# Performance work log

Measured on AMD Instinct MI355X. Metric: run time of the kernel, lower is better.

Reference implementation:

```python
import jax, jax.numpy as jnp
import numpy as np

B, S, D, H, MLP, RH, RANK, BS, E, RES = 64, 197, 768, 12, 3072, 512, 256, 2, 3, 1
EPS = 1e-5


def _ln(x, g, b):
    m = jnp.mean(x, -1, keepdims=True)
    v = jnp.mean((x - m) ** 2, -1, keepdims=True)
    return (x - m) / jnp.sqrt(v + EPS) * g + b


def setup_inputs() -> dict:
    key = jax.random.key(0)
    ks = jax.random.split(key, 16)
    n = lambda k, shp, s: (jax.random.normal(k, shp) * s).astype(jnp.float32)
    inp = {
        'x': n(ks[0], (B, S, D), 1.0),
        'LRA_mask': jnp.arange(2 ** BS, dtype=jnp.int32),
        'wq_w': n(ks[1], (D, D), 0.02), 'wq_b': jnp.zeros((D,), jnp.float32),
        'wk_w': n(ks[2], (D, D), 0.02), 'wk_b': jnp.zeros((D,), jnp.float32),
        'wv_w': n(ks[3], (D, D), 0.02), 'wv_b': jnp.zeros((D,), jnp.float32),
        'wo_w': n(ks[4], (D, D), 0.02), 'wo_b': jnp.zeros((D,), jnp.float32),
        'an_g': jnp.ones((D,), jnp.float32), 'an_b': jnp.zeros((D,), jnp.float32),
        'fc1_w': n(ks[5], (MLP, D), 0.02), 'fc1_b': jnp.zeros((MLP,), jnp.float32),
        'fc2_w': n(ks[6], (D, MLP), 0.02), 'fc2_b': jnp.zeros((D,), jnp.float32),
        'fn_g': jnp.ones((D,), jnp.float32), 'fn_b': jnp.zeros((D,), jnp.float32),
        'r1_w': n(ks[7], (RH, D), 0.01), 'r1_b': jnp.zeros((RH,), jnp.float32),
        'rn_g': jnp.ones((RH,), jnp.float32), 'rn_b': jnp.zeros((RH,), jnp.float32),
        'r2_w': n(ks[8], (BS * 2, RH), 0.01),
        'r2_b': jnp.array([0.1, 5.0] * BS, jnp.float32),
        'eA': n(ks[9], (E, RANK, D), 0.01),  # down_proj weights [out=rank, in=dim]
        'eB': n(ks[10], (E, D, RANK), 0.01),  # up_proj weights [out=dim, in=rank]
    }
    return inp


def reference(x, LRA_mask, wq_w, wq_b, wk_w, wk_b, wv_w, wv_b, wo_w, wo_b,
              an_g, an_b, fc1_w, fc1_b, fc2_w, fc2_b, fn_g, fn_b,
              r1_w, r1_b, rn_g, rn_b, r2_w, r2_b, eA, eB):
    hd = D // H
    # ---- RouterModule (eval mode: argmax hard routing) on block input ----
    rlog = jax.nn.silu(_ln(x @ r1_w.T + r1_b, rn_g, rn_b)) @ r2_w.T + r2_b
    rlog = rlog.reshape(B, S, BS, 2)
    bits = jnp.argmax(rlog, -1)               # [B,S,BS], value of channel-1 one-hot
    bits = bits.at[:, :RES, :].set(1)          # reserved tokens -> full-one key (identity)
    pw = 2 ** jnp.arange(BS - 1, -1, -1)
    idx = jnp.sum(bits * pw, -1)               # [B,S] routing key per token
    # ---- Attention (pre-norm) ----
    h = _ln(x, an_g, an_b)
    q = (h @ wq_w.T + wq_b).reshape(B, S, H, hd).transpose(0, 2, 1, 3)
    k = (h @ wk_w.T + wk_b).reshape(B, S, H, hd).transpose(0, 2, 1, 3)
    v = (h @ wv_w.T + wv_b).reshape(B, S, H, hd).transpose(0, 2, 1, 3)
    att = jax.nn.softmax(jnp.einsum('bhqd,bhkd->bhqk', q, k) / np.float32(np.sqrt(hd)), -1)
    o = jnp.einsum('bhqk,bhkd->bhqd', att, v).transpose(0, 2, 1, 3).reshape(B, S, D)
    x1 = x + (o @ wo_w.T + wo_b)
    # ---- FeedForward (pre-norm, exact GELU like torch nn.GELU) ----
    x2 = x1 + (jax.nn.gelu(_ln(x1, fn_g, fn_b) @ fc1_w.T + fc1_b, approximate=False) @ fc2_w.T + fc2_b)
    # ---- BlockPathApproximators: disjoint per-key residual LoRA experts ----
    # keys 0..E-1 have experts; key 2^BS-1 (full-one) is identity. LRA_mask covers all keys.
    down = jnp.einsum('bsd,erd->bser', x2, eA)            # [B,S,E,RANK]
    up = jnp.einsum('bser,edr->bsed', down, eB)           # [B,S,E,D]
    sel = (idx[..., None] == jnp.arange(E)).astype(x2.dtype)  # one-hot over experts [B,S,E]
    out = x2 + jnp.einsum('bsed,bse->bsd', up, sel)
    return out
```

## Files before the change

### kernel.cpp

```cpp
#include <hip/hip_runtime.h>
#include <cstdint>

#define B_SZ   64
#define SEQ    197
#define DIM    768
#define NHEAD  12
#define HDK    64
#define MLP_D  3072
#define RH_D   512
#define RANK_D 256
#define NEXP   3
#define TOK    (B_SZ*SEQ)

typedef unsigned short u16;
typedef __attribute__((ext_vector_type(8))) short s16x8;
typedef __attribute__((ext_vector_type(4))) float f32x4;

static __device__ __forceinline__ u16 f2bf(float f) {
  unsigned u = __builtin_bit_cast(unsigned, f);
  u = u + 0x7FFFu + ((u >> 16) & 1u);
  return (u16)(u >> 16);
}

static __device__ __forceinline__ f32x4 mfma16(s16x8 a, s16x8 b, f32x4 c) {
  return __builtin_amdgcn_mfma_f32_16x16x32_bf16(a, b, c, 0, 0, 0);
}

static __device__ __forceinline__ void gload16(const u16* g, u16* l) {
  __builtin_amdgcn_global_load_lds(
      (const __attribute__((address_space(1))) unsigned int*)(const void*)g,
      (__attribute__((address_space(3))) unsigned int*)(void*)l,
      16, 0, 0);
}

static __device__ __forceinline__ float gelu_fast(float v) {
  const float u2 = 2.f * v * (0.7978845608f + 0.0356774081f * v * v);
  return v / (1.f + __expf(-u2));
}

__global__ __launch_bounds__(256) void cvt_all(
    const float* __restrict__ s0, const float* __restrict__ s1,
    const float* __restrict__ s2, const float* __restrict__ s3,
    const float* __restrict__ s4, const float* __restrict__ s5,
    const float* __restrict__ s6, const float* __restrict__ s7,
    u16* d0, u16* d1, u16* d2, u16* d3, u16* d4, u16* d5, u16* d6, u16* d7)
{
  const long T4 = 17154048L / 4;
  for (long i = (long)blockIdx.x * 256 + threadIdx.x; i < T4; i += (long)gridDim.x * 256) {
    const long e = i * 4;
    const float* s; u16* d; long off;
    if      (e < 589824L)   { s = s0; d = d0; off = e; }
    else if (e < 1179648L)  { s = s1; d = d1; off = e - 589824L; }
    else if (e < 1769472L)  { s = s2; d = d2; off = e - 1179648L; }
    else if (e < 2359296L)  { s = s3; d = d3; off = e - 1769472L; }
    else if (e < 4718592L)  { s = s4; d = d4; off = e - 2359296L; }
    else if (e < 7077888L)  { s = s5; d = d5; off = e - 4718592L; }
    else if (e < 7471104L)  { s = s6; d = d6; off = e - 7077888L; }
    else                    { s = s7; d = d7; off = e - 7471104L; }
    float4 v = *(const float4*)(s + off);
    unsigned r0 = (unsigned)f2bf(v.x) | ((unsigned)f2bf(v.y) << 16);
    unsigned r1 = (unsigned)f2bf(v.z) | ((unsigned)f2bf(v.w) << 16);
    *(uint2*)(d + off) = make_uint2(r0, r1);
  }
}

__global__ void concat3(const float* __restrict__ a, const float* __restrict__ b,
                        const float* __restrict__ c, float* __restrict__ out) {
  int i = blockIdx.x * 256 + threadIdx.x;
  if (i < DIM) { out[i] = a[i]; out[DIM + i] = b[i]; out[2*DIM + i] = c[i]; }
}

__global__ __launch_bounds__(256) void ln_rows(
    const float* __restrict__ x, const float* __restrict__ g,
    const float* __restrict__ bb, u16* __restrict__ out, int M)
{
  const int row = blockIdx.x * 4 + (threadIdx.x >> 6);
  const int lane = threadIdx.x & 63;
  if (row >= M) return;
  const float* xr = x + (long)row * DIM;
  float4 v[3];
  float s = 0.f, s2 = 0.f;
#pragma unroll
  for (int c = 0; c < 3; ++c) {
    v[c] = *(const float4*)(xr + c*256 + lane*4);
    s  += v[c].x + v[c].y + v[c].z + v[c].w;
    s2 += v[c].x*v[c].x + v[c].y*v[c].y + v[c].z*v[c].z + v[c].w*v[c].w;
  }
#pragma unroll
  for (int o = 1; o < 64; o <<= 1) { s += __shfl_xor(s, o); s2 += __shfl_xor(s2, o); }
  const float mean = s * (1.f/DIM);
  const float var  = s2 * (1.f/DIM) - mean*mean;
  const float rstd = rsqrtf(fmaxf(var, 0.f) + 1e-5f);
#pragma unroll
  for (int c = 0; c < 3; ++c) {
    const int idx = c*256 + lane*4;
    float4 gg = *(const float4*)(g + idx);
    float4 be = *(const float4*)(bb + idx);
    float y0 = (v[c].x - mean)*rstd*gg.x + be.x;
    float y1 = (v[c].y - mean)*rstd*gg.y + be.y;
    float y2 = (v[c].z - mean)*rstd*gg.z + be.z;
    float y3 = (v[c].w - mean)*rstd*gg.w + be.w;
    unsigned r0 = (unsigned)f2bf(y0) | ((unsigned)f2bf(y1) << 16);
    unsigned r1 = (unsigned)f2bf(y2) | ((unsigned)f2bf(y3) << 16);
    *(uint2*)(out + (long)row*DIM + idx) = make_uint2(r0, r1);
  }
}

template<int ACT, bool HAS_RES, bool OUT_F32, bool OUT_BF16>
__global__ __launch_bounds__(256) void gemm_db(
    const u16* __restrict__ A, const u16* __restrict__ Bm,
    const float* __restrict__ bias, const float* __restrict__ res,
    float* __restrict__ Cf, u16* __restrict__ Cb,
    int ldc, int M, int N, int K)
{
  __shared__ __align__(16) u16 lA[2][128*32];
  __shared__ __align__(16) u16 lB[2][128*32];
  const int tid  = threadIdx.x;
  const int lane = tid & 63;
  const int wave = tid >> 6;

  const int nwg  = gridDim.x * gridDim.y;
  const int orig = blockIdx.y * gridDim.x + blockIdx.x;
  const int xcd  = orig & 7;
  const int q    = nwg >> 3, r = nwg & 7;
  const int nb   = (xcd < r ? xcd * (q + 1) : r * (q + 1) + (xcd - r) * q) + (orig >> 3);
  const int m0 = (nb / gridDim.x) * 128;
  const int n0 = (nb % gridDim.x) * 128;

  const int fr = lane & 15, fg = lane >> 4;
  const int wr = wave >> 1, wc = wave & 1;

  const int srow  = tid >> 2;
  const int scol  = (((tid & 3) ^ ((tid >> 3) & 3)) & 3) * 8;
  const int r0a = m0 + srow, r1a = m0 + 64 + srow;
  const u16* pa0 = A  + (long)((r0a < M) ? r0a : M - 1) * K + scol;
  const u16* pa1 = A  + (long)((r1a < M) ? r1a : M - 1) * K + scol;
  const u16* pb0 = Bm + (long)(n0 + srow) * K + scol;
  const u16* pb1 = Bm + (long)(n0 + 64 + srow) * K + scol;
  const int soff = tid * 8;

  auto STAGE = [&](int b, int kt) {
    gload16(pa0 + kt, &lA[b][soff]);
    gload16(pa1 + kt, &lA[b][soff + 2048]);
    gload16(pb0 + kt, &lB[b][soff]);
    gload16(pb1 + kt, &lB[b][soff + 2048]);
  };

  const int abase = fr * 32 + (((fg ^ (fr >> 1)) & 3) << 3);

  f32x4 acc[4][4] = {};
  const int NT = K >> 5;

  STAGE(0, 0);
  __syncthreads();
  int cur = 0;
#pragma unroll 1
  for (int t = 0; t < NT; ++t) {
    if (t + 1 < NT) STAGE(cur ^ 1, (t + 1) << 5);
    s16x8 af[4], bfr[4];
#pragma unroll
    for (int m = 0; m < 4; ++m) af[m]  = *(const s16x8*)&lA[cur][wr*2048 + m*512 + abase];
#pragma unroll
    for (int n = 0; n < 4; ++n) bfr[n] = *(const s16x8*)&lB[cur][wc*2048 + n*512 + abase];
#pragma unroll
    for (int m = 0; m < 4; ++m)
#pragma unroll
      for (int n = 0; n < 4; ++n)
        acc[m][n] = mfma16(af[m], bfr[n], acc[m][n]);
    __syncthreads();
    cur ^= 1;
  }

#pragma unroll
  for (int m = 0; m < 4; ++m) {
#pragma unroll
    for (int n = 0; n < 4; ++n) {
      const int col = n0 + wc*64 + n*16 + fr;
      const float bv = bias[col];
#pragma unroll
      for (int r2 = 0; r2 < 4; ++r2) {
        const int row = m0 + wr*64 + m*16 + fg*4 + r2;
        if (row < M) {
          float v = acc[m][n][r2] + bv;
          if constexpr (ACT == 1) v = gelu_fast(v);
          if constexpr (HAS_RES) v += res[(long)row * N + col];
          if constexpr (OUT_F32) Cf[(long)row * ldc + col] = v;
          if constexpr (OUT_BF16) Cb[(long)row * ldc + col] = f2bf(v);
        }
      }
    }
  }
}

template<int ACT, bool HAS_RES, bool OUT_F32, bool OUT_BF16>
__global__ __launch_bounds__(512) void gemm_wide(
    const u16* __restrict__ A, const u16* __restrict__ Bm,
    const float* __restrict__ bias, const float* __restrict__ res,
    float* __restrict__ Cf, u16* __restrict__ Cb,
    int ldc, int M, int N, int K)
{
  __shared__ __align__(16) u16 lA[2][128*32];
  __shared__ __align__(16) u16 lB[2][256*32];
  const int tid  = threadIdx.x;
  const int lane = tid & 63;
  const int wave = tid >> 6;

  const int nwg  = gridDim.x * gridDim.y;
  const int orig = blockIdx.y * gridDim.x + blockIdx.x;
  const int xcd  = orig & 7;
  const int q    = nwg >> 3, r = nwg & 7;
  const int nb   = (xcd < r ? xcd * (q + 1) : r * (q + 1) + (xcd - r) * q) + (orig >> 3);
  const int m0 = (nb / gridDim.x) * 128;
  const int n0 = (nb % gridDim.x) * 256;

  const int fr = lane & 15, fg = lane >> 4;
  const int wr = wave >> 2, wc = wave & 3;

  const int srow  = tid >> 2;
  const int scol  = (((tid & 3) ^ ((tid >> 3) & 3)) & 3) * 8;
  const int ra = m0 + srow;
  const u16* pa  = A  + (long)((ra < M) ? ra : M - 1) * K + scol;
  const u16* pb0 = Bm + (long)(n0 + srow) * K + scol;
  const u16* pb1 = Bm + (long)(n0 + 128 + srow) * K + scol;
  const int soff = tid * 8;

  auto STAGE = [&](int b, int kt) {
    gload16(pa  + kt, &lA[b][soff]);
    gload16(pb0 + kt, &lB[b][soff]);
    gload16(pb1 + kt, &lB[b][soff + 4096]);
  };

  const int abase = fr * 32 + (((fg ^ (fr >> 1)) & 3) << 3);

  f32x4 acc[4][4] = {};
  const int NT = K >> 5;

  STAGE(0, 0);
  __syncthreads();
  int cur = 0;
#pragma unroll 1
  for (int t = 0; t < NT; ++t) {
    if (t + 1 < NT) STAGE(cur ^ 1, (t + 1) << 5);
    s16x8 af[4], bfr[4];
#pragma unroll
    for (int m = 0; m < 4; ++m) af[m]  = *(const s16x8*)&lA[cur][wr*2048 + m*512 + abase];
#pragma unroll
    for (int n = 0; n < 4; ++n) bfr[n] = *(const s16x8*)&lB[cur][wc*2048 + n*512 + abase];
#pragma unroll
    for (int m = 0; m < 4; ++m)
#pragma unroll
      for (int n = 0; n < 4; ++n)
        acc[m][n] = mfma16(af[m], bfr[n], acc[m][n]);
    __syncthreads();
    cur ^= 1;
  }

#pragma unroll
  for (int m = 0; m < 4; ++m) {
#pragma unroll
    for (int n = 0; n < 4; ++n) {
      const int col = n0 + wc*64 + n*16 + fr;
      const float bv = bias[col];
#pragma unroll
      for (int r2 = 0; r2 < 4; ++r2) {
        const int row = m0 + wr*64 + m*16 + fg*4 + r2;
        if (row < M) {
          float v = acc[m][n][r2] + bv;
          if constexpr (ACT == 1) v = gelu_fast(v);
          if constexpr (HAS_RES) v += res[(long)row * N + col];
          if constexpr (OUT_F32) Cf[(long)row * ldc + col] = v;
          if constexpr (OUT_BF16) Cb[(long)row * ldc + col] = f2bf(v);
        }
      }
    }
  }
}

__global__ __launch_bounds__(256, 2) void attn(const u16* __restrict__ qkv, u16* __restrict__ o) {
  __shared__ __align__(16) u16 Vt[64][232];
  __shared__ __align__(16) u16 Pl[4][16][232];
  const int bh = blockIdx.x;
  const int b = bh / NHEAD, h = bh - b * NHEAD;
  const int tid = threadIdx.x, lane = tid & 63, wave = tid >> 6;
  const long rbase = (long)b * SEQ * 2304;

  for (int i = tid; i < 224*64; i += 256) {
    const int s = i >> 6, d = i & 63;
    u16 val = 0;
    if (s < SEQ) val = qkv[rbase + (long)s*2304 + 1536 + h*HDK + d];
    Vt[d][s] = val;
  }
  for (int i = lane; i < 16*24; i += 64) {
    Pl[wave][i / 24][208 + i % 24] = 0;
  }
  __syncthreads();

  const int fr = lane & 15, fg = lane >> 4;
  for (int qb = wave; qb < 13; qb += 4) {
    const int q0 = qb * 16;
    int qrow = q0 + fr; if (qrow > SEQ-1) qrow = SEQ-1;
    const u16* qp = qkv + rbase + (long)qrow*2304 + h*HDK;
    const s16x8 a0 = *(const s16x8*)(qp + fg*8);
    const s16x8 a1 = *(const s16x8*)(qp + 32 + fg*8);
    f32x4 sc[13];
    for (int kb = 0; kb < 13; ++kb) {
      int krow = kb*16 + fr; if (krow > SEQ-1) krow = SEQ-1;
      const u16* kp = qkv + rbase + (long)krow*2304 + DIM + h*HDK;
      const s16x8 b0 = *(const s16x8*)(kp + fg*8);
      const s16x8 b1 = *(const s16x8*)(kp + 32 + fg*8);
      f32x4 c = {0.f, 0.f, 0.f, 0.f};
      c = mfma16(a0, b0, c);
      c = mfma16(a1, b1, c);
      sc[kb] = c;
    }
    float inv[4];
#pragma unroll
    for (int r = 0; r < 4; ++r) {
      float mx = -3e38f;
      for (int kb = 0; kb < 13; ++kb) {
        const int col = kb*16 + fr;
        const float sv = sc[kb][r] * 0.125f;
        sc[kb][r] = sv;
        if (col < SEQ) mx = fmaxf(mx, sv);
      }
#pragma unroll
      for (int off = 1; off < 16; off <<= 1) mx = fmaxf(mx, __shfl_xor(mx, off));
      float sum = 0.f;
      for (int kb = 0; kb < 13; ++kb) {
        const int col = kb*16 + fr;
        const float p = (col < SEQ) ? __expf(sc[kb][r] - mx) : 0.f;
        sc[kb][r] = p;
        sum += p;
      }
#pragma unroll
      for (int off = 1; off < 16; off <<= 1) sum += __shfl_xor(sum, off);
      inv[r] = 1.f / sum;
    }
    asm volatile("s_waitcnt lgkmcnt(0)" ::: "memory");
    for (int kb = 0; kb < 13; ++kb) {
      const int col = kb*16 + fr;
#pragma unroll
      for (int r = 0; r < 4; ++r) Pl[wave][fg*4 + r][col] = f2bf(sc[kb][r]);
    }
    asm volatile("s_waitcnt lgkmcnt(0)" ::: "memory");
    for (int nb2 = 0; nb2 < 4; ++nb2) {
      f32x4 acc = {0.f, 0.f, 0.f, 0.f};
#pragma unroll
      for (int kc = 0; kc < 7; ++kc) {
        const s16x8 pa = *(const s16x8*)&Pl[wave][fr][kc*32 + fg*8];
        const s16x8 vb = *(const s16x8*)&Vt[nb2*16 + fr][kc*32 + fg*8];
        acc = mfma16(pa, vb, acc);
      }
#pragma unroll
      for (int r = 0; r < 4; ++r) {
        const int qr = q0 + fg*4 + r;
        if (qr < SEQ) o[((long)b*SEQ + qr)*DIM + h*HDK + nb2*16 + fr] = f2bf(acc[r] * inv[r]);
      }
    }
  }
}

__global__ __launch_bounds__(64) void router_fin(
    const float* __restrict__ t1, const float* __restrict__ rg, const float* __restrict__ rb,
    const float* __restrict__ r2w, const float* __restrict__ r2b, int* __restrict__ idxb)
{
  const int t = blockIdx.x;
  const int lane = threadIdx.x;
  const float* row = t1 + (long)t * RH_D;
  float v[8];
  float s = 0.f, s2 = 0.f;
#pragma unroll
  for (int c = 0; c < 2; ++c) {
    float4 u = *(const float4*)(row + lane*8 + c*4);
    v[c*4+0]=u.x; v[c*4+1]=u.y; v[c*4+2]=u.z; v[c*4+3]=u.w;
    s += u.x+u.y+u.z+u.w;
    s2 += u.x*u.x+u.y*u.y+u.z*u.z+u.w*u.w;
  }
#pragma unroll
  for (int o = 1; o < 64; o <<= 1) { s += __shfl_xor(s, o); s2 += __shfl_xor(s2, o); }
  const float mean = s * (1.f/RH_D);
  const float var  = s2 * (1.f/RH_D) - mean*mean;
  const float rstd = rsqrtf(fmaxf(var, 0.f) + 1e-5f);
  float p[4] = {0.f, 0.f, 0.f, 0.f};
#pragma unroll
  for (int i = 0; i < 8; ++i) {
    const int col = lane*8 + i;
    float z = (v[i] - mean)*rstd*rg[col] + rb[col];
    z = z / (1.f + __expf(-z));
#pragma unroll
    for (int o = 0; o < 4; ++o) p[o] += z * r2w[o*RH_D + col];
  }
#pragma unroll
  for (int o = 0; o < 4; ++o)
#pragma unroll
    for (int off = 1; off < 64; off <<= 1) p[o] += __shfl_xor(p[o], off);
  if (lane == 0) {
    const float l0 = p[0]+r2b[0], l1 = p[1]+r2b[1], l2 = p[2]+r2b[2], l3 = p[3]+r2b[3];
    int b0 = (l1 > l0) ? 1 : 0;
    int b1 = (l3 > l2) ? 1 : 0;
    if (t % SEQ < 1) { b0 = 1; b1 = 1; }
    idxb[t] = b0*2 + b1;
  }
}

__global__ __launch_bounds__(256) void expert_apply(
    const int* __restrict__ idxb, const float* __restrict__ eA,
    const float* __restrict__ eB, float* __restrict__ out)
{
  const int t = blockIdx.x;
  const int e = idxb[t];
  if (e >= NEXP) return;
  __shared__ float xr[DIM];
  __shared__ float dn[RANK_D];
  const int tid = threadIdx.x;
  for (int i = tid; i < DIM; i += 256) xr[i] = out[(long)t*DIM + i];
  __syncthreads();
  {
    const float* ar = eA + ((long)e*RANK_D + tid)*DIM;
    float acc = 0.f;
    for (int k = 0; k < DIM; ++k) acc += ar[k]*xr[k];
    dn[tid] = acc;
  }
  __syncthreads();
  for (int d = tid; d < DIM; d += 256) {
    const float* br = eB + ((long)e*DIM + d)*RANK_D;
    float acc = 0.f;
    for (int r = 0; r < RANK_D; ++r) acc += br[r]*dn[r];
    out[(long)t*DIM + d] += acc;
  }
}

extern "C" void kernel_launch(void* const* d_in, const int* in_sizes, int n_in,
                              void* d_out, int out_size, void* d_ws, size_t ws_size,
                              hipStream_t stream) {
  (void)in_sizes; (void)n_in; (void)out_size;
  const float* x     = (const float*)d_in[0];
  const float* wq_w  = (const float*)d_in[2];
  const float* wq_b  = (const float*)d_in[3];
  const float* wk_w  = (const float*)d_in[4];
  const float* wk_b  = (const float*)d_in[5];
  const float* wv_w  = (const float*)d_in[6];
  const float* wv_b  = (const float*)d_in[7];
  const float* wo_w  = (const float*)d_in[8];
  const float* wo_b  = (const float*)d_in[9];
  const float* an_g  = (const float*)d_in[10];
  const float* an_b  = (const float*)d_in[11];
  const float* fc1_w = (const float*)d_in[12];
  const float* fc1_b = (const float*)d_in[13];
  const float* fc2_w = (const float*)d_in[14];
  const float* fc2_b = (const float*)d_in[15];
  const float* fn_g  = (const float*)d_in[16];
  const float* fn_b  = (const float*)d_in[17];
  const float* r1_w  = (const float*)d_in[18];
  const float* r1_b  = (const float*)d_in[19];
  const float* rn_g  = (const float*)d_in[20];
  const float* rn_b  = (const float*)d_in[21];
  const float* r2_w  = (const float*)d_in[22];
  const float* r2_b  = (const float*)d_in[23];
  const float* eA    = (const float*)d_in[24];
  const float* eB    = (const float*)d_in[25];
  float* outf = (float*)d_out;

  const size_t MiB = 1048576;
  const size_t NEED_FULL = 153*MiB;
  const size_t NEED_MIN  = 112*MiB + (size_t)TOK*DIM*2;
  if (ws_size < NEED_MIN) return;
  const bool full = (ws_size >= NEED_FULL);
  const int  nc   = full ? 1 : 2;
  const int  MC   = TOK / nc;
  const size_t offSY = full ? 94*MiB  : 72*MiB;
  const size_t offSZ = full ? 133*MiB : 112*MiB;

  char* ws = (char*)d_ws;
  u16*   Wqkv = (u16*)(ws + 0);
  u16*   Wo   = (u16*)(ws + 3538944);
  u16*   Wfc1 = (u16*)(ws + 4718592);
  u16*   Wfc2 = (u16*)(ws + 9437184);
  u16*   Wr1  = (u16*)(ws + 14155776);
  float* qkvb = (float*)(ws + 14942208);
  int*   idxb = (int*)(ws + 14952448);
  char* SX = ws + 16*MiB;
  char* SY = ws + offSY;
  char* SZ = ws + offSZ;
  u16*   x_b = (u16*)SX;
  u16*   qkv = (u16*)SX;
  u16*   m1  = (u16*)SX;
  float* t1  = (float*)SY;
  float* x1  = (float*)SY;
  u16*   h_b = (u16*)SZ;
  u16*   ob  = (u16*)SZ;
  u16*   h1  = (u16*)SZ;

  cvt_all<<<2048, 256, 0, stream>>>(
      wq_w, wk_w, wv_w, wo_w, fc1_w, fc2_w, r1_w, x,
      Wqkv, Wqkv + 589824, Wqkv + 2*589824, Wo, Wfc1, Wfc2, Wr1, x_b);
  concat3<<<3, 256, 0, stream>>>(wq_b, wk_b, wv_b, qkvb);

  gemm_db<0, false, true, false><<<dim3(4, 99), 256, 0, stream>>>(
      x_b, Wr1, r1_b, nullptr, t1, nullptr, RH_D, TOK, RH_D, DIM);
  router_fin<<<TOK, 64, 0, stream>>>(t1, rn_g, rn_b, r2_w, r2_b, idxb);

  ln_rows<<<TOK/4, 256, 0, stream>>>(x, an_g, an_b, h_b, TOK);
  gemm_wide<0, false, false, true><<<dim3(9, 99), 512, 0, stream>>>(
      h_b, Wqkv, qkvb, nullptr, nullptr, qkv, 3*DIM, TOK, 3*DIM, DIM);
  attn<<<B_SZ*NHEAD, 256, 0, stream>>>(qkv, ob);
  gemm_db<0, true, true, false><<<dim3(6, 99), 256, 0, stream>>>(
      ob, Wo, wo_b, x, x1, nullptr, DIM, TOK, DIM, DIM);

  ln_rows<<<TOK/4, 256, 0, stream>>>(x1, fn_g, fn_b, h1, TOK);
  for (int c = 0; c < nc; ++c) {
    const int r0 = c * MC;
    const int gy = (MC + 127) / 128;
    gemm_wide<1, false, false, true><<<dim3(12, gy), 512, 0, stream>>>(
        h1 + (long)r0*DIM, Wfc1, fc1_b, nullptr, nullptr, m1, MLP_D, MC, MLP_D, DIM);
    gemm_db<0, true, true, false><<<dim3(6, gy), 256, 0, stream>>>(
        m1, Wfc2, fc2_b, x1 + (long)r0*DIM, outf + (long)r0*DIM, nullptr, DIM, MC, DIM, MLP_D);
  }

  expert_apply<<<TOK, 256, 0, stream>>>(idxb, eA, eB, outf);
}
```

Before: 432.1 us.

## Enlarge wide GEMM tile to 256x256 and fuse x bf16 cast into LayerNorm

The 512-thread GEMM used for QKV and fc1 now computes 256x256 output tiles, with each wave holding 8x4 MFMA accumulators instead of 4x4. This raises arithmetic intensity and halves the grid along M. The bf16 conversion of x moves out of the weight-cast kernel into the first LayerNorm pass, which already reads x, so x is read one fewer time. The bigger tile roughly doubles LDS and accumulator register use, which may lower occupancy and leave more tail imbalance with fewer workgroups.

```diff
diff --git a/kernel.cpp b/kernel.cpp
--- a/kernel.cpp
+++ b/kernel.cpp
@@ -42,10 +42,10 @@
     const float* __restrict__ s0, const float* __restrict__ s1,
     const float* __restrict__ s2, const float* __restrict__ s3,
     const float* __restrict__ s4, const float* __restrict__ s5,
-    const float* __restrict__ s6, const float* __restrict__ s7,
-    u16* d0, u16* d1, u16* d2, u16* d3, u16* d4, u16* d5, u16* d6, u16* d7)
+    const float* __restrict__ s6,
+    u16* d0, u16* d1, u16* d2, u16* d3, u16* d4, u16* d5, u16* d6)
 {
-  const long T4 = 17154048L / 4;
+  const long T4 = 7471104L / 4;
   for (long i = (long)blockIdx.x * 256 + threadIdx.x; i < T4; i += (long)gridDim.x * 256) {
     const long e = i * 4;
     const float* s; u16* d; long off;
@@ -55,8 +55,7 @@
     else if (e < 2359296L)  { s = s3; d = d3; off = e - 1769472L; }
     else if (e < 4718592L)  { s = s4; d = d4; off = e - 2359296L; }
     else if (e < 7077888L)  { s = s5; d = d5; off = e - 4718592L; }
-    else if (e < 7471104L)  { s = s6; d = d6; off = e - 7077888L; }
-    else                    { s = s7; d = d7; off = e - 7471104L; }
+    else                    { s = s6; d = d6; off = e - 7077888L; }
     float4 v = *(const float4*)(s + off);
     unsigned r0 = (unsigned)f2bf(v.x) | ((unsigned)f2bf(v.y) << 16);
     unsigned r1 = (unsigned)f2bf(v.z) | ((unsigned)f2bf(v.w) << 16);
@@ -72,7 +71,8 @@
 
 __global__ __launch_bounds__(256) void ln_rows(
     const float* __restrict__ x, const float* __restrict__ g,
-    const float* __restrict__ bb, u16* __restrict__ out, int M)
+    const float* __restrict__ bb, u16* __restrict__ out,
+    u16* __restrict__ out_raw, int M)
 {
   const int row = blockIdx.x * 4 + (threadIdx.x >> 6);
   const int lane = threadIdx.x & 63;
@@ -103,6 +103,11 @@
     unsigned r0 = (unsigned)f2bf(y0) | ((unsigned)f2bf(y1) << 16);
     unsigned r1 = (unsigned)f2bf(y2) | ((unsigned)f2bf(y3) << 16);
     *(uint2*)(out + (long)row*DIM + idx) = make_uint2(r0, r1);
+    if (out_raw) {
+      unsigned q0 = (unsigned)f2bf(v[c].x) | ((unsigned)f2bf(v[c].y) << 16);
+      unsigned q1 = (unsigned)f2bf(v[c].z) | ((unsigned)f2bf(v[c].w) << 16);
+      *(uint2*)(out_raw + (long)row*DIM + idx) = make_uint2(q0, q1);
+    }
   }
 }
 
@@ -193,13 +198,13 @@
 }
 
 template<int ACT, bool HAS_RES, bool OUT_F32, bool OUT_BF16>
-__global__ __launch_bounds__(512) void gemm_wide(
+__global__ __launch_bounds__(512) void gemm_big(
     const u16* __restrict__ A, const u16* __restrict__ Bm,
     const float* __restrict__ bias, const float* __restrict__ res,
     float* __restrict__ Cf, u16* __restrict__ Cb,
     int ldc, int M, int N, int K)
 {
-  __shared__ __align__(16) u16 lA[2][128*32];
+  __shared__ __align__(16) u16 lA[2][256*32];
   __shared__ __align__(16) u16 lB[2][256*32];
   const int tid  = threadIdx.x;
   const int lane = tid & 63;
@@ -210,29 +215,31 @@
   const int xcd  = orig & 7;
   const int q    = nwg >> 3, r = nwg & 7;
   const int nb   = (xcd < r ? xcd * (q + 1) : r * (q + 1) + (xcd - r) * q) + (orig >> 3);
-  const int m0 = (nb / gridDim.x) * 128;
+  const int m0 = (nb / gridDim.x) * 256;
   const int n0 = (nb % gridDim.x) * 256;
 
   const int fr = lane & 15, fg = lane >> 4;
-  const int wr = wave >> 2, wc = wave & 3;
+  const int wr = wave >> 2, wcol = wave & 3;
 
   const int srow  = tid >> 2;
   const int scol  = (((tid & 3) ^ ((tid >> 3) & 3)) & 3) * 8;
-  const int ra = m0 + srow;
-  const u16* pa  = A  + (long)((ra < M) ? ra : M - 1) * K + scol;
+  const int r0a = m0 + srow, r1a = m0 + 128 + srow;
+  const u16* pa0 = A  + (long)((r0a < M) ? r0a : M - 1) * K + scol;
+  const u16* pa1 = A  + (long)((r1a < M) ? r1a : M - 1) * K + scol;
   const u16* pb0 = Bm + (long)(n0 + srow) * K + scol;
   const u16* pb1 = Bm + (long)(n0 + 128 + srow) * K + scol;
   const int soff = tid * 8;
 
   auto STAGE = [&](int b, int kt) {
-    gload16(pa  + kt, &lA[b][soff]);
+    gload16(pa0 + kt, &lA[b][soff]);
+    gload16(pa1 + kt, &lA[b][soff + 4096]);
     gload16(pb0 + kt, &lB[b][soff]);
     gload16(pb1 + kt, &lB[b][soff + 4096]);
   };
 
   const int abase = fr * 32 + (((fg ^ (fr >> 1)) & 3) << 3);
 
-  f32x4 acc[4][4] = {};
+  f32x4 acc[8][4] = {};
   const int NT = K >> 5;
 
   STAGE(0, 0);
@@ -241,13 +248,13 @@
 #pragma unroll 1
   for (int t = 0; t < NT; ++t) {
     if (t + 1 < NT) STAGE(cur ^ 1, (t + 1) << 5);
-    s16x8 af[4], bfr[4];
-#pragma unroll
-    for (int m = 0; m < 4; ++m) af[m]  = *(const s16x8*)&lA[cur][wr*2048 + m*512 + abase];
-#pragma unroll
-    for (int n = 0; n < 4; ++n) bfr[n] = *(const s16x8*)&lB[cur][wc*2048 + n*512 + abase];
-#pragma unroll
-    for (int m = 0; m < 4; ++m)
+    s16x8 af[8], bfr[4];
+#pragma unroll
+    for (int m = 0; m < 8; ++m) af[m]  = *(const s16x8*)&lA[cur][wr*4096 + m*512 + abase];
+#pragma unroll
+    for (int n = 0; n < 4; ++n) bfr[n] = *(const s16x8*)&lB[cur][wcol*2048 + n*512 + abase];
+#pragma unroll
+    for (int m = 0; m < 8; ++m)
 #pragma unroll
       for (int n = 0; n < 4; ++n)
         acc[m][n] = mfma16(af[m], bfr[n], acc[m][n]);
@@ -256,14 +263,14 @@
   }
 
 #pragma unroll
-  for (int m = 0; m < 4; ++m) {
+  for (int m = 0; m < 8; ++m) {
 #pragma unroll
     for (int n = 0; n < 4; ++n) {
-      const int col = n0 + wc*64 + n*16 + fr;
+      const int col = n0 + wcol*64 + n*16 + fr;
       const float bv = bias[col];
 #pragma unroll
       for (int r2 = 0; r2 < 4; ++r2) {
-        const int row = m0 + wr*64 + m*16 + fg*4 + r2;
+        const int row = m0 + wr*128 + m*16 + fg*4 + r2;
         if (row < M) {
           float v = acc[m][n][r2] + bv;
           if constexpr (ACT == 1) v = gelu_fast(v);
@@ -491,29 +498,31 @@
   u16*   ob  = (u16*)SZ;
   u16*   h1  = (u16*)SZ;
 
-  cvt_all<<<2048, 256, 0, stream>>>(
-      wq_w, wk_w, wv_w, wo_w, fc1_w, fc2_w, r1_w, x,
-      Wqkv, Wqkv + 589824, Wqkv + 2*589824, Wo, Wfc1, Wfc2, Wr1, x_b);
+  cvt_all<<<1024, 256, 0, stream>>>(
+      wq_w, wk_w, wv_w, wo_w, fc1_w, fc2_w, r1_w,
+      Wqkv, Wqkv + 589824, Wqkv + 2*589824, Wo, Wfc1, Wfc2, Wr1);
   concat3<<<3, 256, 0, stream>>>(wq_b, wk_b, wv_b, qkvb);
+
+  ln_rows<<<TOK/4, 256, 0, stream>>>(x, an_g, an_b, h_b, x_b, TOK);
 
   gemm_db<0, false, true, false><<<dim3(4, 99), 256, 0, stream>>>(
       x_b, Wr1, r1_b, nullptr, t1, nullptr, RH_D, TOK, RH_D, DIM);
   router_fin<<<TOK, 64, 0, stream>>>(t1, rn_g, rn_b, r2_w, r2_b, idxb);
 
-  ln_rows<<<TOK/4, 256, 0, stream>>>(x, an_g, an_b, h_b, TOK);
-  gemm_wide<0, false, false, true><<<dim3(9, 99), 512, 0, stream>>>(
+  gemm_big<0, false, false, true><<<dim3(9, 50), 512, 0, stream>>>(
       h_b, Wqkv, qkvb, nullptr, nullptr, qkv, 3*DIM, TOK, 3*DIM, DIM);
   attn<<<B_SZ*NHEAD, 256, 0, stream>>>(qkv, ob);
   gemm_db<0, true, true, false><<<dim3(6, 99), 256, 0, stream>>>(
       ob, Wo, wo_b, x, x1, nullptr, DIM, TOK, DIM, DIM);
 
-  ln_rows<<<TOK/4, 256, 0, stream>>>(x1, fn_g, fn_b, h1, TOK);
+  ln_rows<<<TOK/4, 256, 0, stream>>>(x1, fn_g, fn_b, h1, nullptr, TOK);
   for (int c = 0; c < nc; ++c) {
     const int r0 = c * MC;
-    const int gy = (MC + 127) / 128;
-    gemm_wide<1, false, false, true><<<dim3(12, gy), 512, 0, stream>>>(
+    const int gyb = (MC + 255) / 256;
+    const int gyd = (MC + 127) / 128;
+    gemm_big<1, false, false, true><<<dim3(12, gyb), 512, 0, stream>>>(
         h1 + (long)r0*DIM, Wfc1, fc1_b, nullptr, nullptr, m1, MLP_D, MC, MLP_D, DIM);
-    gemm_db<0, true, true, false><<<dim3(6, gy), 256, 0, stream>>>(
+    gemm_db<0, true, true, false><<<dim3(6, gyd), 256, 0, stream>>>(
         m1, Wfc2, fc2_b, x1 + (long)r0*DIM, outf + (long)r0*DIM, nullptr, DIM, MC, DIM, MLP_D);
   }
 
```

Result: slower. 493.3 us (+14.2%).
